# Kernel optimization log

Hardware: AMD Instinct MI355X
Metric: run time of the kernel (lower is better)

## Reference

```python
import jax, jax.numpy as jnp
import numpy as np

NUM_EXPERTS = 8
TOP_K = 2
ROUTED_SCALE = 1.0  # routed_scaling_factor
D_MODEL = 2048
D_FFN = 1408


def setup_inputs() -> dict:
    key = jax.random.key(0)
    ks = jax.random.split(key, 8)
    s = 0.02  # init scale for weights
    return {
        'hidden_states': jax.random.normal(ks[0], (2, 1024, D_MODEL), jnp.float32),
        'gate_w': jax.random.normal(ks[1], (NUM_EXPERTS, D_MODEL), jnp.float32) * s,
        'w_gate': jax.random.normal(ks[2], (NUM_EXPERTS, D_MODEL, D_FFN), jnp.float32) * s,
        'w_up': jax.random.normal(ks[3], (NUM_EXPERTS, D_MODEL, D_FFN), jnp.float32) * s,
        'w_down': jax.random.normal(ks[4], (NUM_EXPERTS, D_FFN, D_MODEL), jnp.float32) * s,
        'sw_gate': jax.random.normal(ks[5], (D_MODEL, D_FFN), jnp.float32) * s,
        'sw_up': jax.random.normal(ks[6], (D_MODEL, D_FFN), jnp.float32) * s,
        'sw_down': jax.random.normal(ks[7], (D_FFN, D_MODEL), jnp.float32) * s,
    }


def reference(hidden_states, gate_w, w_gate, w_up, w_down, sw_gate, sw_up, sw_down):
    B, S, D = hidden_states.shape
    x = hidden_states.reshape(-1, D)            # [T, D]
    T = x.shape[0]

    # --- router: fp32 linear -> softmax -> top-k -> renormalize ---
    logits = jnp.einsum('td,ed->te', x.astype(jnp.float32), gate_w)   # [T, E]
    probs = jax.nn.softmax(logits, axis=-1)
    topk_w, topk_ids = jax.lax.top_k(probs, TOP_K)                    # [T, K]
    topk_w = topk_w / jnp.sum(topk_w, axis=-1, keepdims=True)         # norm_topk_prob
    # dense per-token expert gates [T, E] (zero for unselected experts)
    gates = jnp.zeros((T, NUM_EXPERTS), jnp.float32).at[
        jnp.arange(T)[:, None], topk_ids].add(topk_w)
    gates = gates.astype(x.dtype)

    # --- routed experts: SwiGLU per expert, masked dense combine ---
    g = jnp.einsum('td,edf->etf', x, w_gate)    # [E, T, F]
    u = jnp.einsum('td,edf->etf', x, w_up)      # [E, T, F]
    h = jax.nn.silu(g) * u                      # SiluAndMul
    down = jnp.einsum('etf,efd->etd', h, w_down)  # [E, T, D]
    routed = jnp.einsum('te,etd->td', gates, down)  # combine
    routed = routed * ROUTED_SCALE

    # --- shared expert MLP ---
    shared = (jax.nn.silu(x @ sw_gate) * (x @ sw_up)) @ sw_down

    out = routed + shared
    return out.reshape(B, S, D)
```

## Files before the change

### kernel.cpp

```cpp
#include <hip/hip_runtime.h>
#include <hip/hip_bf16.h>

#define T_TOK 2048
#define DM    2048
#define FF    1408
#define NE    8
#define MT_ROUTED 40
#define MT_TOTAL  56
#define ROUTED_CAP 5120
#define NSLOT 7168

typedef unsigned short u16;
typedef __attribute__((ext_vector_type(4))) u16 u16x4;
typedef __attribute__((ext_vector_type(8))) short bf16x8;
typedef __attribute__((ext_vector_type(4))) float f32x4;

__device__ __forceinline__ u16 f2bf(float f) {
    unsigned u = __float_as_uint(f);
    unsigned r = (u + 0x7FFFu + ((u >> 16) & 1u)) >> 16;
    return (u16)r;
}

__device__ __forceinline__ void gll16(const void* g, void* l) {
    __builtin_amdgcn_global_load_lds((const __attribute__((address_space(1))) void*)g,
                                     (__attribute__((address_space(3))) void*)l, 16, 0, 0);
}

constexpr size_t SZ_XB  = (size_t)T_TOK * DM * 2;
constexpr size_t SZ_WE  = (size_t)NE * DM * FF * 2;
constexpr size_t SZ_SW  = (size_t)DM * FF * 2;
constexpr size_t SZ_H   = (size_t)NSLOT * FF * 2;
constexpr size_t SZ_DN  = (size_t)NSLOT * DM * 4;

constexpr size_t OFF_XB   = 0;
constexpr size_t OFF_WGT  = OFF_XB + SZ_XB;
constexpr size_t OFF_WUT  = OFF_WGT + SZ_WE;
constexpr size_t OFF_WDT  = OFF_WUT + SZ_WE;
constexpr size_t OFF_SWG  = OFF_WDT + SZ_WE;
constexpr size_t OFF_SWU  = OFF_SWG + SZ_SW;
constexpr size_t OFF_SWD  = OFF_SWU + SZ_SW;
constexpr size_t OFF_H    = OFF_SWD + SZ_SW;
constexpr size_t OFF_DN   = OFF_H + SZ_H;
constexpr size_t OFF_TID  = OFF_DN + SZ_DN;
constexpr size_t OFF_TW   = OFF_TID + (size_t)T_TOK*2*4;
constexpr size_t OFF_PERM = OFF_TW  + (size_t)T_TOK*2*4;
constexpr size_t OFF_SW_S = OFF_PERM + (size_t)ROUTED_CAP*4;
constexpr size_t OFF_TKS  = OFF_SW_S + (size_t)ROUTED_CAP*4;
constexpr size_t OFF_TE   = OFF_TKS + (size_t)T_TOK*2*4;

__global__ void cvtx_kernel(const float* __restrict__ src, u16* __restrict__ dst) {
    const int i = blockIdx.x * 256 + threadIdx.x;
    const float4 v = ((const float4*)src)[i];
    u16x4 o; o.x = f2bf(v.x); o.y = f2bf(v.y); o.z = f2bf(v.z); o.w = f2bf(v.w);
    ((u16x4*)dst)[i] = o;
}

__global__ void tcvt64_kernel(const float* __restrict__ src, u16* __restrict__ dst, int R, int C) {
    __shared__ u16 tile[64][72];
    const size_t msz = (size_t)R * C;
    const float* s = src + (size_t)blockIdx.z * msz;
    u16* d = dst + (size_t)blockIdx.z * msz;
    const int r0 = blockIdx.y * 64, c0 = blockIdx.x * 64;
    const int tr = threadIdx.x >> 4, tc = (threadIdx.x & 15) * 4;
#pragma unroll
    for (int i = 0; i < 4; i++) {
        const int r = tr + i * 16;
        const float4 v = *(const float4*)(s + (size_t)(r0 + r) * C + (c0 + tc));
        tile[r][tc+0] = f2bf(v.x); tile[r][tc+1] = f2bf(v.y);
        tile[r][tc+2] = f2bf(v.z); tile[r][tc+3] = f2bf(v.w);
    }
    __syncthreads();
#pragma unroll
    for (int i = 0; i < 4; i++) {
        const int c = tr + i * 16;
        u16x4 o;
        o.x = tile[tc+0][c]; o.y = tile[tc+1][c]; o.z = tile[tc+2][c]; o.w = tile[tc+3][c];
        *(u16x4*)(d + (size_t)(c0 + c) * R + (r0 + tc)) = o;
    }
}

__global__ void router_kernel(const float* __restrict__ x, const float* __restrict__ gw,
                              int* __restrict__ topk_id, float* __restrict__ topk_w) {
    const int wv = threadIdx.x >> 6, l = threadIdx.x & 63;
    const int t = blockIdx.x * 4 + wv;
    const float* xt = x + (size_t)t * DM;
    float acc[NE] = {0.f,0.f,0.f,0.f,0.f,0.f,0.f,0.f};
    for (int d = l * 4; d < DM; d += 256) {
        const float4 xv = *(const float4*)(xt + d);
#pragma unroll
        for (int e = 0; e < NE; e++) {
            const float4 w4 = *(const float4*)(gw + e * DM + d);
            acc[e] += xv.x * w4.x + xv.y * w4.y + xv.z * w4.z + xv.w * w4.w;
        }
    }
#pragma unroll
    for (int e = 0; e < NE; e++)
#pragma unroll
        for (int off = 32; off > 0; off >>= 1) acc[e] += __shfl_xor(acc[e], off, 64);
    if (l == 0) {
        float m = acc[0];
#pragma unroll
        for (int e = 1; e < NE; e++) m = fmaxf(m, acc[e]);
        float p[NE];
#pragma unroll
        for (int e = 0; e < NE; e++) p[e] = __expf(acc[e] - m);
        int i1 = 0; float b1 = p[0];
#pragma unroll
        for (int e = 1; e < NE; e++) if (p[e] > b1) { b1 = p[e]; i1 = e; }
        int i2 = -1; float b2 = -1.f;
#pragma unroll
        for (int e = 0; e < NE; e++) if (e != i1 && p[e] > b2) { b2 = p[e]; i2 = e; }
        const float s = b1 + b2;
        topk_id[2*t] = i1; topk_id[2*t+1] = i2;
        topk_w[2*t] = b1 / s; topk_w[2*t+1] = b2 / s;
    }
}

__global__ void scan_kernel(const int* __restrict__ topk_id, const float* __restrict__ topk_w,
                            int* __restrict__ perm_token, float* __restrict__ slot_w,
                            int* __restrict__ tk_slot, int* __restrict__ tile_e) {
    const int e = blockIdx.x;
    const int tid = threadIdx.x;
    __shared__ int cnt[NE];
    __shared__ int tsum[256];
    int ids[16];
#pragma unroll
    for (int j = 0; j < 16; j++) ids[j] = topk_id[tid * 16 + j];
    if (tid < NE) cnt[tid] = 0;
    __syncthreads();
#pragma unroll
    for (int e2 = 0; e2 < NE; e2++) {
        int c = 0;
#pragma unroll
        for (int j = 0; j < 16; j++) c += (ids[j] == e2);
        if (c) atomicAdd(&cnt[e2], c);
    }
    int mySum = 0;
#pragma unroll
    for (int j = 0; j < 16; j++) mySum += (ids[j] == e);
    tsum[tid] = mySum;
    __syncthreads();
    if (tid == 0) { int run = 0; for (int i = 0; i < 256; i++) { int v = tsum[i]; tsum[i] = run; run += v; } }
    __syncthreads();
    int poff = 0;
#pragma unroll
    for (int e2 = 0; e2 < NE; e2++) { int p = (cnt[e2] + 127) & ~127; if (e2 < e) poff += p; }
    const int padded_e = (cnt[e] + 127) & ~127;
    int run = tsum[tid];
#pragma unroll
    for (int j = 0; j < 16; j++) {
        if (ids[j] == e) {
            const int i = tid * 16 + j;
            const int slot = poff + run;
            perm_token[slot] = i >> 1;
            slot_w[slot] = topk_w[i];
            tk_slot[i] = slot;
            run++;
        }
    }
    for (int r = cnt[e] + tid; r < padded_e; r += 256) { perm_token[poff + r] = 0; slot_w[poff + r] = 0.f; }
    if (tid == 0) for (int tt = poff >> 7; tt < (poff + padded_e) >> 7; tt++) tile_e[tt] = e;
    if (e == 0 && tid == 1) {
        int ptot = 0;
#pragma unroll
        for (int e2 = 0; e2 < NE; e2++) ptot += (cnt[e2] + 127) & ~127;
        for (int tt = ptot >> 7; tt < MT_ROUTED; tt++) tile_e[tt] = -1;
        for (int tt = MT_ROUTED; tt < MT_TOTAL; tt++) tile_e[tt] = 8;
    }
}

__global__ __launch_bounds__(256, 2)
void gemm1_kernel(const u16* __restrict__ xb,
                  const u16* __restrict__ wgT, const u16* __restrict__ wuT,
                  const u16* __restrict__ swgT, const u16* __restrict__ swuT,
                  const int* __restrict__ perm_token, const float* __restrict__ slot_w,
                  const int* __restrict__ tile_e, u16* __restrict__ hbuf) {
    const int mtile = blockIdx.y, ntile = blockIdx.x;
    const int e = tile_e[mtile];
    if (e < 0) return;
    __shared__ u16 lA[128 * 64], lBg[128 * 64], lBu[128 * 64];
    __shared__ int lTok[128];
    __shared__ float lW[128];
    const int tid = threadIdx.x, l = tid & 63, w = tid >> 6;
    const bool sh = (e == 8);
    const int slot_base = sh ? (ROUTED_CAP + (mtile - MT_ROUTED) * 128) : mtile * 128;
    if (tid < 128) {
        if (sh) { lTok[tid] = (mtile - MT_ROUTED) * 128 + tid; lW[tid] = 1.0f; }
        else {
            int tok = perm_token[slot_base + tid];
            lTok[tid] = (tok < 0) ? 0 : tok;
            lW[tid] = slot_w[slot_base + tid];
        }
    }
    __syncthreads();
    const u16* Bg = sh ? swgT : (wgT + (size_t)e * FF * DM);
    const u16* Bu = sh ? swuT : (wuT + (size_t)e * FF * DM);
    const int n0 = ntile * 128;
    const u16* aSrc[4]; const u16* bgSrc[4]; const u16* buSrc[4]; int ldsOff[4];
#pragma unroll
    for (int i = 0; i < 4; i++) {
        const int row = i * 32 + w * 8 + (l >> 3);
        const int ch = (l & 7) ^ (row & 7);
        ldsOff[i] = (i * 32 + w * 8) * 64;
        aSrc[i]  = xb + (size_t)lTok[row] * DM + ch * 8;
        bgSrc[i] = Bg + (size_t)(n0 + row) * DM + ch * 8;
        buSrc[i] = Bu + (size_t)(n0 + row) * DM + ch * 8;
    }
    f32x4 accg[4][4] = {}; f32x4 accu[4][4] = {};
    const int wm = (w >> 1) * 64, wn = (w & 1) * 64;
    for (int k0 = 0; k0 < DM; k0 += 64) {
        __syncthreads();
#pragma unroll
        for (int i = 0; i < 4; i++) {
            gll16(aSrc[i] + k0, lA + ldsOff[i]);
            gll16(bgSrc[i] + k0, lBg + ldsOff[i]);
            gll16(buSrc[i] + k0, lBu + ldsOff[i]);
        }
        __syncthreads();
#pragma unroll
        for (int kk = 0; kk < 64; kk += 32) {
            bf16x8 af[4], bgf[4], buf2[4];
#pragma unroll
            for (int mi = 0; mi < 4; mi++) {
                const int row = wm + mi * 16 + (l & 15);
                const int ch = ((kk >> 3) + (l >> 4)) ^ (row & 7);
                af[mi] = *(const bf16x8*)(lA + row * 64 + ch * 8);
            }
#pragma unroll
            for (int ni = 0; ni < 4; ni++) {
                const int row = wn + ni * 16 + (l & 15);
                const int ch = ((kk >> 3) + (l >> 4)) ^ (row & 7);
                bgf[ni]  = *(const bf16x8*)(lBg + row * 64 + ch * 8);
                buf2[ni] = *(const bf16x8*)(lBu + row * 64 + ch * 8);
            }
#pragma unroll
            for (int mi = 0; mi < 4; mi++)
#pragma unroll
                for (int ni = 0; ni < 4; ni++) {
                    accg[mi][ni] = __builtin_amdgcn_mfma_f32_16x16x32_bf16(af[mi], bgf[ni], accg[mi][ni], 0, 0, 0);
                    accu[mi][ni] = __builtin_amdgcn_mfma_f32_16x16x32_bf16(af[mi], buf2[ni], accu[mi][ni], 0, 0, 0);
                }
        }
    }
#pragma unroll
    for (int mi = 0; mi < 4; mi++) {
#pragma unroll
        for (int r = 0; r < 4; r++) {
            const int m = wm + mi * 16 + (l >> 4) * 4 + r;
            const float wgt = lW[m];
#pragma unroll
            for (int ni = 0; ni < 4; ni++) {
                const int n = wn + ni * 16 + (l & 15);
                const float g = accg[mi][ni][r], u = accu[mi][ni][r];
                const float h = g * (1.f / (1.f + __expf(-g))) * u * wgt;
                hbuf[(size_t)(slot_base + m) * FF + n0 + n] = f2bf(h);
            }
        }
    }
}

__global__ __launch_bounds__(256, 2)
void gemm2_kernel(const u16* __restrict__ hbuf, const u16* __restrict__ wdT,
                  const u16* __restrict__ swdT, const int* __restrict__ tile_e,
                  float* __restrict__ dn) {
    const int mtile = blockIdx.y, ntile = blockIdx.x;
    const int e = tile_e[mtile];
    if (e < 0) return;
    __shared__ u16 lA[128 * 64], lB[128 * 64];
    const int tid = threadIdx.x, l = tid & 63, w = tid >> 6;
    const bool sh = (e == 8);
    const int slot_base = sh ? (ROUTED_CAP + (mtile - MT_ROUTED) * 128) : mtile * 128;
    const u16* Bp = sh ? swdT : (wdT + (size_t)e * DM * FF);
    const int n0 = ntile * 128;
    const u16* aSrc[4]; const u16* bSrc[4]; int ldsOff[4];
#pragma unroll
    for (int i = 0; i < 4; i++) {
        const int row = i * 32 + w * 8 + (l >> 3);
        const int ch = (l & 7) ^ (row & 7);
        ldsOff[i] = (i * 32 + w * 8) * 64;
        aSrc[i] = hbuf + (size_t)(slot_base + row) * FF + ch * 8;
        bSrc[i] = Bp + (size_t)(n0 + row) * FF + ch * 8;
    }
    f32x4 acc[4][4] = {};
    const int wm = (w >> 1) * 64, wn = (w & 1) * 64;
    for (int k0 = 0; k0 < FF; k0 += 64) {
        __syncthreads();
#pragma unroll
        for (int i = 0; i < 4; i++) { gll16(aSrc[i] + k0, lA + ldsOff[i]); gll16(bSrc[i] + k0, lB + ldsOff[i]); }
        __syncthreads();
#pragma unroll
        for (int kk = 0; kk < 64; kk += 32) {
            bf16x8 af[4], bf_[4];
#pragma unroll
            for (int mi = 0; mi < 4; mi++) {
                const int row = wm + mi * 16 + (l & 15);
                const int ch = ((kk >> 3) + (l >> 4)) ^ (row & 7);
                af[mi] = *(const bf16x8*)(lA + row * 64 + ch * 8);
            }
#pragma unroll
            for (int ni = 0; ni < 4; ni++) {
                const int row = wn + ni * 16 + (l & 15);
                const int ch = ((kk >> 3) + (l >> 4)) ^ (row & 7);
                bf_[ni] = *(const bf16x8*)(lB + row * 64 + ch * 8);
            }
#pragma unroll
            for (int mi = 0; mi < 4; mi++)
#pragma unroll
                for (int ni = 0; ni < 4; ni++)
                    acc[mi][ni] = __builtin_amdgcn_mfma_f32_16x16x32_bf16(af[mi], bf_[ni], acc[mi][ni], 0, 0, 0);
        }
    }
#pragma unroll
    for (int mi = 0; mi < 4; mi++)
#pragma unroll
        for (int r = 0; r < 4; r++) {
            const int m = wm + mi * 16 + (l >> 4) * 4 + r;
#pragma unroll
            for (int ni = 0; ni < 4; ni++) {
                const int n = wn + ni * 16 + (l & 15);
                dn[(size_t)(slot_base + m) * DM + n0 + n] = acc[mi][ni][r];
            }
        }
}

__global__ void combine_kernel(const float* __restrict__ dn, const int* __restrict__ tk_slot,
                               float* __restrict__ out) {
    const int i = blockIdx.x * 256 + threadIdx.x;
    const int base = i * 4;
    const int t = base >> 11, d = base & 2047;
    const int s1 = tk_slot[2 * t], s2 = tk_slot[2 * t + 1];
    const float4 a = *(const float4*)(dn + (size_t)s1 * DM + d);
    const float4 b = *(const float4*)(dn + (size_t)s2 * DM + d);
    const float4 c = *(const float4*)(dn + (size_t)(ROUTED_CAP + t) * DM + d);
    float4 o;
    o.x = a.x + b.x + c.x; o.y = a.y + b.y + c.y;
    o.z = a.z + b.z + c.z; o.w = a.w + b.w + c.w;
    *(float4*)(out + base) = o;
}

extern "C" void kernel_launch(void* const* d_in, const int* in_sizes, int n_in,
                              void* d_out, int out_size, void* d_ws, size_t ws_size,
                              hipStream_t stream) {
    (void)in_sizes; (void)n_in; (void)out_size; (void)ws_size;
    const float* x   = (const float*)d_in[0];
    const float* gw  = (const float*)d_in[1];
    const float* wg  = (const float*)d_in[2];
    const float* wu  = (const float*)d_in[3];
    const float* wd  = (const float*)d_in[4];
    const float* swg = (const float*)d_in[5];
    const float* swu = (const float*)d_in[6];
    const float* swd = (const float*)d_in[7];
    float* out = (float*)d_out;
    char* ws = (char*)d_ws;

    u16*   xb    = (u16*)(ws + OFF_XB);
    u16*   wgT   = (u16*)(ws + OFF_WGT);
    u16*   wuT   = (u16*)(ws + OFF_WUT);
    u16*   wdT   = (u16*)(ws + OFF_WDT);
    u16*   swgT  = (u16*)(ws + OFF_SWG);
    u16*   swuT  = (u16*)(ws + OFF_SWU);
    u16*   swdT  = (u16*)(ws + OFF_SWD);
    u16*   hbuf  = (u16*)(ws + OFF_H);
    float* dn    = (float*)(ws + OFF_DN);
    int*   tid_  = (int*)(ws + OFF_TID);
    float* tw    = (float*)(ws + OFF_TW);
    int*   perm  = (int*)(ws + OFF_PERM);
    float* slw   = (float*)(ws + OFF_SW_S);
    int*   tks   = (int*)(ws + OFF_TKS);
    int*   te    = (int*)(ws + OFF_TE);

    cvtx_kernel<<<(T_TOK * DM / 4) / 256, 256, 0, stream>>>(x, xb);
    tcvt64_kernel<<<dim3(FF / 64, DM / 64, NE), 256, 0, stream>>>(wg, wgT, DM, FF);
    tcvt64_kernel<<<dim3(FF / 64, DM / 64, NE), 256, 0, stream>>>(wu, wuT, DM, FF);
    tcvt64_kernel<<<dim3(DM / 64, FF / 64, NE), 256, 0, stream>>>(wd, wdT, FF, DM);
    tcvt64_kernel<<<dim3(FF / 64, DM / 64, 1), 256, 0, stream>>>(swg, swgT, DM, FF);
    tcvt64_kernel<<<dim3(FF / 64, DM / 64, 1), 256, 0, stream>>>(swu, swuT, DM, FF);
    tcvt64_kernel<<<dim3(DM / 64, FF / 64, 1), 256, 0, stream>>>(swd, swdT, FF, DM);
    router_kernel<<<T_TOK / 4, 256, 0, stream>>>(x, gw, tid_, tw);
    scan_kernel<<<NE, 256, 0, stream>>>(tid_, tw, perm, slw, tks, te);
    gemm1_kernel<<<dim3(FF / 128, MT_TOTAL), 256, 0, stream>>>(xb, wgT, wuT, swgT, swuT, perm, slw, te, hbuf);
    gemm2_kernel<<<dim3(DM / 128, MT_TOTAL), 256, 0, stream>>>(hbuf, wdT, swdT, te, dn);
    combine_kernel<<<(T_TOK * DM / 4) / 256, 256, 0, stream>>>(dn, tks, out);
}
```

Before: 343.4 us.

## Fuse conversion launches, shrink GEMM tiles, and store down-proj output in bf16

```diff
diff --git a/kernel.cpp b/kernel.cpp
--- a/kernel.cpp
+++ b/kernel.cpp
@@ -20,6 +20,9 @@
     unsigned r = (u + 0x7FFFu + ((u >> 16) & 1u)) >> 16;
     return (u16)r;
 }
+__device__ __forceinline__ float bf2f(u16 v) {
+    return __uint_as_float(((unsigned)v) << 16);
+}
 
 __device__ __forceinline__ void gll16(const void* g, void* l) {
     __builtin_amdgcn_global_load_lds((const __attribute__((address_space(1))) void*)g,
@@ -30,7 +33,7 @@
 constexpr size_t SZ_WE  = (size_t)NE * DM * FF * 2;
 constexpr size_t SZ_SW  = (size_t)DM * FF * 2;
 constexpr size_t SZ_H   = (size_t)NSLOT * FF * 2;
-constexpr size_t SZ_DN  = (size_t)NSLOT * DM * 4;
+constexpr size_t SZ_DN  = (size_t)NSLOT * DM * 2;
 
 constexpr size_t OFF_XB   = 0;
 constexpr size_t OFF_WGT  = OFF_XB + SZ_XB;
@@ -48,18 +51,19 @@
 constexpr size_t OFF_TKS  = OFF_SW_S + (size_t)ROUTED_CAP*4;
 constexpr size_t OFF_TE   = OFF_TKS + (size_t)T_TOK*2*4;
 
-__global__ void cvtx_kernel(const float* __restrict__ src, u16* __restrict__ dst) {
-    const int i = blockIdx.x * 256 + threadIdx.x;
-    const float4 v = ((const float4*)src)[i];
-    u16x4 o; o.x = f2bf(v.x); o.y = f2bf(v.y); o.z = f2bf(v.z); o.w = f2bf(v.w);
-    ((u16x4*)dst)[i] = o;
-}
-
-__global__ void tcvt64_kernel(const float* __restrict__ src, u16* __restrict__ dst, int R, int C) {
+__global__ void tcvtA_kernel(const float* __restrict__ wg, const float* __restrict__ wu,
+                             const float* __restrict__ swg, const float* __restrict__ swu,
+                             u16* __restrict__ wgT, u16* __restrict__ wuT,
+                             u16* __restrict__ swgT, u16* __restrict__ swuT) {
     __shared__ u16 tile[64][72];
-    const size_t msz = (size_t)R * C;
-    const float* s = src + (size_t)blockIdx.z * msz;
-    u16* d = dst + (size_t)blockIdx.z * msz;
+    const int z = blockIdx.z;
+    const size_t msz = (size_t)DM * FF;
+    const float* s; u16* d;
+    if (z < 8)       { s = wg + (size_t)z * msz;        d = wgT + (size_t)z * msz; }
+    else if (z < 16) { s = wu + (size_t)(z - 8) * msz;  d = wuT + (size_t)(z - 8) * msz; }
+    else if (z == 16){ s = swg;                          d = swgT; }
+    else             { s = swu;                          d = swuT; }
+    const int R = DM, C = FF;
     const int r0 = blockIdx.y * 64, c0 = blockIdx.x * 64;
     const int tr = threadIdx.x >> 4, tc = (threadIdx.x & 15) * 4;
 #pragma unroll
@@ -79,14 +83,46 @@
     }
 }
 
+__global__ void tcvtB_kernel(const float* __restrict__ wd, const float* __restrict__ swd,
+                             u16* __restrict__ wdT, u16* __restrict__ swdT) {
+    __shared__ u16 tile[64][72];
+    const int z = blockIdx.z;
+    const size_t msz = (size_t)DM * FF;
+    const float* s; u16* d;
+    if (z < 8) { s = wd + (size_t)z * msz; d = wdT + (size_t)z * msz; }
+    else       { s = swd;                  d = swdT; }
+    const int R = FF, C = DM;
+    const int r0 = blockIdx.y * 64, c0 = blockIdx.x * 64;
+    const int tr = threadIdx.x >> 4, tc = (threadIdx.x & 15) * 4;
+#pragma unroll
+    for (int i = 0; i < 4; i++) {
+        const int r = tr + i * 16;
+        const float4 v = *(const float4*)(s + (size_t)(r0 + r) * C + (c0 + tc));
+        tile[r][tc+0] = f2bf(v.x); tile[r][tc+1] = f2bf(v.y);
+        tile[r][tc+2] = f2bf(v.z); tile[r][tc+3] = f2bf(v.w);
+    }
+    __syncthreads();
+#pragma unroll
+    for (int i = 0; i < 4; i++) {
+        const int c = tr + i * 16;
+        u16x4 o;
+        o.x = tile[tc+0][c]; o.y = tile[tc+1][c]; o.z = tile[tc+2][c]; o.w = tile[tc+3][c];
+        *(u16x4*)(d + (size_t)(c0 + c) * R + (r0 + tc)) = o;
+    }
+}
+
 __global__ void router_kernel(const float* __restrict__ x, const float* __restrict__ gw,
+                              u16* __restrict__ xb,
                               int* __restrict__ topk_id, float* __restrict__ topk_w) {
     const int wv = threadIdx.x >> 6, l = threadIdx.x & 63;
     const int t = blockIdx.x * 4 + wv;
     const float* xt = x + (size_t)t * DM;
+    u16* xbt = xb + (size_t)t * DM;
     float acc[NE] = {0.f,0.f,0.f,0.f,0.f,0.f,0.f,0.f};
     for (int d = l * 4; d < DM; d += 256) {
         const float4 xv = *(const float4*)(xt + d);
+        u16x4 o; o.x = f2bf(xv.x); o.y = f2bf(xv.y); o.z = f2bf(xv.z); o.w = f2bf(xv.w);
+        *(u16x4*)(xbt + d) = o;
 #pragma unroll
         for (int e = 0; e < NE; e++) {
             const float4 w4 = *(const float4*)(gw + e * DM + d);
@@ -169,7 +205,7 @@
     }
 }
 
-__global__ __launch_bounds__(256, 2)
+__global__ __launch_bounds__(256, 3)
 void gemm1_kernel(const u16* __restrict__ xb,
                   const u16* __restrict__ wgT, const u16* __restrict__ wuT,
                   const u16* __restrict__ swgT, const u16* __restrict__ swuT,
@@ -178,7 +214,7 @@
     const int mtile = blockIdx.y, ntile = blockIdx.x;
     const int e = tile_e[mtile];
     if (e < 0) return;
-    __shared__ u16 lA[128 * 64], lBg[128 * 64], lBu[128 * 64];
+    __shared__ u16 lA[128 * 64], lB[128 * 64];
     __shared__ int lTok[128];
     __shared__ float lW[128];
     const int tid = threadIdx.x, l = tid & 63, w = tid >> 6;
@@ -195,147 +231,153 @@
     __syncthreads();
     const u16* Bg = sh ? swgT : (wgT + (size_t)e * FF * DM);
     const u16* Bu = sh ? swuT : (wuT + (size_t)e * FF * DM);
-    const int n0 = ntile * 128;
-    const u16* aSrc[4]; const u16* bgSrc[4]; const u16* buSrc[4]; int ldsOff[4];
+    const int n0 = ntile * 64;
+    const u16* aSrc[4]; const u16* bSrc[4]; int ldsOff[4];
 #pragma unroll
     for (int i = 0; i < 4; i++) {
         const int row = i * 32 + w * 8 + (l >> 3);
         const int ch = (l & 7) ^ (row & 7);
         ldsOff[i] = (i * 32 + w * 8) * 64;
-        aSrc[i]  = xb + (size_t)lTok[row] * DM + ch * 8;
-        bgSrc[i] = Bg + (size_t)(n0 + row) * DM + ch * 8;
-        buSrc[i] = Bu + (size_t)(n0 + row) * DM + ch * 8;
-    }
-    f32x4 accg[4][4] = {}; f32x4 accu[4][4] = {};
-    const int wm = (w >> 1) * 64, wn = (w & 1) * 64;
+        aSrc[i] = xb + (size_t)lTok[row] * DM + ch * 8;
+        const u16* bbase = (i < 2) ? (Bg + (size_t)(n0 + row) * DM)
+                                   : (Bu + (size_t)(n0 + row - 64) * DM);
+        bSrc[i] = bbase + ch * 8;
+    }
+    f32x4 acc[2][8] = {};
+    const int wm = w * 32;
     for (int k0 = 0; k0 < DM; k0 += 64) {
         __syncthreads();
 #pragma unroll
-        for (int i = 0; i < 4; i++) {
-            gll16(aSrc[i] + k0, lA + ldsOff[i]);
-            gll16(bgSrc[i] + k0, lBg + ldsOff[i]);
-            gll16(buSrc[i] + k0, lBu + ldsOff[i]);
-        }
+        for (int i = 0; i < 4; i++) { gll16(aSrc[i] + k0, lA + ldsOff[i]); gll16(bSrc[i] + k0, lB + ldsOff[i]); }
         __syncthreads();
 #pragma unroll
         for (int kk = 0; kk < 64; kk += 32) {
-            bf16x8 af[4], bgf[4], buf2[4];
-#pragma unroll
-            for (int mi = 0; mi < 4; mi++) {
+            bf16x8 af[2], bf_[8];
+#pragma unroll
+            for (int mi = 0; mi < 2; mi++) {
                 const int row = wm + mi * 16 + (l & 15);
                 const int ch = ((kk >> 3) + (l >> 4)) ^ (row & 7);
                 af[mi] = *(const bf16x8*)(lA + row * 64 + ch * 8);
             }
 #pragma unroll
-            for (int ni = 0; ni < 4; ni++) {
-                const int row = wn + ni * 16 + (l & 15);
+            for (int ni = 0; ni < 8; ni++) {
+                const int row = ni * 16 + (l & 15);
                 const int ch = ((kk >> 3) + (l >> 4)) ^ (row & 7);
-                bgf[ni]  = *(const bf16x8*)(lBg + row * 64 + ch * 8);
-                buf2[ni] = *(const bf16x8*)(lBu + row * 64 + ch * 8);
-            }
-#pragma unroll
-            for (int mi = 0; mi < 4; mi++)
-#pragma unroll
-                for (int ni = 0; ni < 4; ni++) {
-                    accg[mi][ni] = __builtin_amdgcn_mfma_f32_16x16x32_bf16(af[mi], bgf[ni], accg[mi][ni], 0, 0, 0);
-                    accu[mi][ni] = __builtin_amdgcn_mfma_f32_16x16x32_bf16(af[mi], buf2[ni], accu[mi][ni], 0, 0, 0);
-                }
-        }
-    }
-#pragma unroll
-    for (int mi = 0; mi < 4; mi++) {
+                bf_[ni] = *(const bf16x8*)(lB + row * 64 + ch * 8);
+            }
+#pragma unroll
+            for (int mi = 0; mi < 2; mi++)
+#pragma unroll
+                for (int ni = 0; ni < 8; ni++)
+                    acc[mi][ni] = __builtin_amdgcn_mfma_f32_16x16x32_bf16(af[mi], bf_[ni], acc[mi][ni], 0, 0, 0);
+        }
+    }
+#pragma unroll
+    for (int mi = 0; mi < 2; mi++)
 #pragma unroll
         for (int r = 0; r < 4; r++) {
             const int m = wm + mi * 16 + (l >> 4) * 4 + r;
             const float wgt = lW[m];
 #pragma unroll
             for (int ni = 0; ni < 4; ni++) {
-                const int n = wn + ni * 16 + (l & 15);
-                const float g = accg[mi][ni][r], u = accu[mi][ni][r];
+                const int n = ni * 16 + (l & 15);
+                const float g = acc[mi][ni][r], u = acc[mi][ni + 4][r];
                 const float h = g * (1.f / (1.f + __expf(-g))) * u * wgt;
                 hbuf[(size_t)(slot_base + m) * FF + n0 + n] = f2bf(h);
             }
         }
-    }
-}
-
-__global__ __launch_bounds__(256, 2)
+}
+
+__global__ __launch_bounds__(256, 4)
 void gemm2_kernel(const u16* __restrict__ hbuf, const u16* __restrict__ wdT,
                   const u16* __restrict__ swdT, const int* __restrict__ tile_e,
-                  float* __restrict__ dn) {
+                  u16* __restrict__ dn) {
     const int mtile = blockIdx.y, ntile = blockIdx.x;
     const int e = tile_e[mtile];
     if (e < 0) return;
-    __shared__ u16 lA[128 * 64], lB[128 * 64];
+    __shared__ u16 lA[128 * 64], lB[64 * 64];
     const int tid = threadIdx.x, l = tid & 63, w = tid >> 6;
     const bool sh = (e == 8);
     const int slot_base = sh ? (ROUTED_CAP + (mtile - MT_ROUTED) * 128) : mtile * 128;
     const u16* Bp = sh ? swdT : (wdT + (size_t)e * DM * FF);
-    const int n0 = ntile * 128;
-    const u16* aSrc[4]; const u16* bSrc[4]; int ldsOff[4];
+    const int n0 = ntile * 64;
+    const u16* aSrc[4]; const u16* bSrc[2]; int ldsOffA[4]; int ldsOffB[2];
 #pragma unroll
     for (int i = 0; i < 4; i++) {
         const int row = i * 32 + w * 8 + (l >> 3);
         const int ch = (l & 7) ^ (row & 7);
-        ldsOff[i] = (i * 32 + w * 8) * 64;
+        ldsOffA[i] = (i * 32 + w * 8) * 64;
         aSrc[i] = hbuf + (size_t)(slot_base + row) * FF + ch * 8;
+    }
+#pragma unroll
+    for (int i = 0; i < 2; i++) {
+        const int row = i * 32 + w * 8 + (l >> 3);
+        const int ch = (l & 7) ^ (row & 7);
+        ldsOffB[i] = (i * 32 + w * 8) * 64;
         bSrc[i] = Bp + (size_t)(n0 + row) * FF + ch * 8;
     }
-    f32x4 acc[4][4] = {};
-    const int wm = (w >> 1) * 64, wn = (w & 1) * 64;
+    f32x4 acc[2][4] = {};
+    const int wm = w * 32;
     for (int k0 = 0; k0 < FF; k0 += 64) {
         __syncthreads();
 #pragma unroll
-        for (int i = 0; i < 4; i++) { gll16(aSrc[i] + k0, lA + ldsOff[i]); gll16(bSrc[i] + k0, lB + ldsOff[i]); }
+        for (int i = 0; i < 4; i++) gll16(aSrc[i] + k0, lA + ldsOffA[i]);
+#pragma unroll
+        for (int i = 0; i < 2; i++) gll16(bSrc[i] + k0, lB + ldsOffB[i]);
         __syncthreads();
 #pragma unroll
         for (int kk = 0; kk < 64; kk += 32) {
-            bf16x8 af[4], bf_[4];
-#pragma unroll
-            for (int mi = 0; mi < 4; mi++) {
+            bf16x8 af[2], bf_[4];
+#pragma unroll
+            for (int mi = 0; mi < 2; mi++) {
                 const int row = wm + mi * 16 + (l & 15);
                 const int ch = ((kk >> 3) + (l >> 4)) ^ (row & 7);
                 af[mi] = *(const bf16x8*)(lA + row * 64 + ch * 8);
             }
 #pragma unroll
             for (int ni = 0; ni < 4; ni++) {
-                const int row = wn + ni * 16 + (l & 15);
+                const int row = ni * 16 + (l & 15);
                 const int ch = ((kk >> 3) + (l >> 4)) ^ (row & 7);
                 bf_[ni] = *(const bf16x8*)(lB + row * 64 + ch * 8);
             }
 #pragma unroll
-            for (int mi = 0; mi < 4; mi++)
+            for (int mi = 0; mi < 2; mi++)
 #pragma unroll
                 for (int ni = 0; ni < 4; ni++)
                     acc[mi][ni] = __builtin_amdgcn_mfma_f32_16x16x32_bf16(af[mi], bf_[ni], acc[mi][ni], 0, 0, 0);
         }
     }
 #pragma unroll
-    for (int mi = 0; mi < 4; mi++)
+    for (int mi = 0; mi < 2; mi++)
 #pragma unroll
         for (int r = 0; r < 4; r++) {
             const int m = wm + mi * 16 + (l >> 4) * 4 + r;
 #pragma unroll
             for (int ni = 0; ni < 4; ni++) {
-                const int n = wn + ni * 16 + (l & 15);
-                dn[(size_t)(slot_base + m) * DM + n0 + n] = acc[mi][ni][r];
-            }
-        }
-}
-
-__global__ void combine_kernel(const float* __restrict__ dn, const int* __restrict__ tk_slot,
+                const int n = ni * 16 + (l & 15);
+                dn[(size_t)(slot_base + m) * DM + n0 + n] = f2bf(acc[mi][ni][r]);
+            }
+        }
+}
+
+__global__ void combine_kernel(const u16* __restrict__ dn, const int* __restrict__ tk_slot,
                                float* __restrict__ out) {
     const int i = blockIdx.x * 256 + threadIdx.x;
-    const int base = i * 4;
+    const int base = i * 8;
     const int t = base >> 11, d = base & 2047;
     const int s1 = tk_slot[2 * t], s2 = tk_slot[2 * t + 1];
-    const float4 a = *(const float4*)(dn + (size_t)s1 * DM + d);
-    const float4 b = *(const float4*)(dn + (size_t)s2 * DM + d);
-    const float4 c = *(const float4*)(dn + (size_t)(ROUTED_CAP + t) * DM + d);
-    float4 o;
-    o.x = a.x + b.x + c.x; o.y = a.y + b.y + c.y;
-    o.z = a.z + b.z + c.z; o.w = a.w + b.w + c.w;
-    *(float4*)(out + base) = o;
+    const bf16x8 a = *(const bf16x8*)(dn + (size_t)s1 * DM + d);
+    const bf16x8 b = *(const bf16x8*)(dn + (size_t)s2 * DM + d);
+    const bf16x8 c = *(const bf16x8*)(dn + (size_t)(ROUTED_CAP + t) * DM + d);
+    float o[8];
+#pragma unroll
+    for (int j = 0; j < 8; j++)
+        o[j] = bf2f((u16)a[j]) + bf2f((u16)b[j]) + bf2f((u16)c[j]);
+    float4 lo, hi;
+    lo.x = o[0]; lo.y = o[1]; lo.z = o[2]; lo.w = o[3];
+    hi.x = o[4]; hi.y = o[5]; hi.z = o[6]; hi.w = o[7];
+    *(float4*)(out + base) = lo;
+    *(float4*)(out + base + 4) = hi;
 }
 
 extern "C" void kernel_launch(void* const* d_in, const int* in_sizes, int n_in,
@@ -361,7 +403,7 @@
     u16*   swuT  = (u16*)(ws + OFF_SWU);
     u16*   swdT  = (u16*)(ws + OFF_SWD);
     u16*   hbuf  = (u16*)(ws + OFF_H);
-    float* dn    = (float*)(ws + OFF_DN);
+    u16*   dn    = (u16*)(ws + OFF_DN);
     int*   tid_  = (int*)(ws + OFF_TID);
     float* tw    = (float*)(ws + OFF_TW);
     int*   perm  = (int*)(ws + OFF_PERM);
@@ -369,16 +411,11 @@
     int*   tks   = (int*)(ws + OFF_TKS);
     int*   te    = (int*)(ws + OFF_TE);
 
-    cvtx_kernel<<<(T_TOK * DM / 4) / 256, 256, 0, stream>>>(x, xb);
-    tcvt64_kernel<<<dim3(FF / 64, DM / 64, NE), 256, 0, stream>>>(wg, wgT, DM, FF);
-    tcvt64_kernel<<<dim3(FF / 64, DM / 64, NE), 256, 0, stream>>>(wu, wuT, DM, FF);
-    tcvt64_kernel<<<dim3(DM / 64, FF / 64, NE), 256, 0, stream>>>(wd, wdT, FF, DM);
-    tcvt64_kernel<<<dim3(FF / 64, DM / 64, 1), 256, 0, stream>>>(swg, swgT, DM, FF);
-    tcvt64_kernel<<<dim3(FF / 64, DM / 64, 1), 256, 0, stream>>>(swu, swuT, DM, FF);
-    tcvt64_kernel<<<dim3(DM / 64, FF / 64, 1), 256, 0, stream>>>(swd, swdT, FF, DM);
-    router_kernel<<<T_TOK / 4, 256, 0, stream>>>(x, gw, tid_, tw);
+    router_kernel<<<T_TOK / 4, 256, 0, stream>>>(x, gw, xb, tid_, tw);
     scan_kernel<<<NE, 256, 0, stream>>>(tid_, tw, perm, slw, tks, te);
-    gemm1_kernel<<<dim3(FF / 128, MT_TOTAL), 256, 0, stream>>>(xb, wgT, wuT, swgT, swuT, perm, slw, te, hbuf);
-    gemm2_kernel<<<dim3(DM / 128, MT_TOTAL), 256, 0, stream>>>(hbuf, wdT, swdT, te, dn);
-    combine_kernel<<<(T_TOK * DM / 4) / 256, 256, 0, stream>>>(dn, tks, out);
-}
+    tcvtA_kernel<<<dim3(FF / 64, DM / 64, 18), 256, 0, stream>>>(wg, wu, swg, swu, wgT, wuT, swgT, swuT);
+    tcvtB_kernel<<<dim3(DM / 64, FF / 64, 9), 256, 0, stream>>>(wd, swd, wdT, swdT);
+    gemm1_kernel<<<dim3(FF / 64, MT_TOTAL), 256, 0, stream>>>(xb, wgT, wuT, swgT, swuT, perm, slw, te, hbuf);
+    gemm2_kernel<<<dim3(DM / 64, MT_TOTAL), 256, 0, stream>>>(hbuf, wdT, swdT, te, dn);
+    combine_kernel<<<(T_TOK * DM / 8) / 256, 256, 0, stream>>>(dn, tks, out);
+}
```

New measurement: 293.4 us. -14.6%, faster.
